# Kernel optimization log

Hardware: AMD Instinct MI355X
Metric: run time of the kernel (lower is better)

## Reference

```python
import jax, jax.numpy as jnp
import numpy as np

NOTRACK_BOX = jnp.array([-1.0, -1.0, -1.0, -1.0], dtype=jnp.float32)
ROI_SIZE = 7


def make_boxes(key, B, N):
    k1, k2 = jax.random.split(key)
    lo = jax.random.uniform(k1, (B, N, 2)) * 0.5            # (ymin, xmin)
    sz = jax.random.uniform(k2, (B, N, 2)) * 0.45 + 0.05    # box extent
    hi = jnp.minimum(lo + sz, 1.0)
    boxes = jnp.concatenate([lo, hi], axis=-1)               # [B,N,4] ymin,xmin,ymax,xmax
    # mark last 2 slots per batch as empty (NOTRACK_BOX)
    boxes = boxes.at[:, -2:, :].set(-1.0)
    return boxes


def setup_inputs() -> dict:
    key = jax.random.key(0)
    ks = jax.random.split(key, 6)
    B, H, W, N, C, D = 16, 512, 512, 16, 256, 256
    images = jax.random.normal(ks[0], (B, H, W, 3), dtype=jnp.float32)
    bboxes = make_boxes(ks[1], B, N)
    conv_w = jax.random.normal(ks[2], (16, 16, 3, C), dtype=jnp.float32) * 0.05
    conv_b = jnp.zeros((C,), dtype=jnp.float32)
    dense_w = jax.random.normal(ks[3], (C, D), dtype=jnp.float32) * (1.0 / np.sqrt(C))
    dense_b = jnp.zeros((D,), dtype=jnp.float32)
    return {"images": images, "bboxes": bboxes, "conv_w": conv_w,
            "conv_b": conv_b, "dense_w": dense_w, "dense_b": dense_b}


def backbone(images, conv_w, conv_b):
    # stride-16 conv stem: [B,512,512,3] -> [B,32,32,C]
    feat = jax.lax.conv_general_dilated(
        images, conv_w, window_strides=(16, 16), padding="VALID",
        dimension_numbers=("NHWC", "HWIO", "NHWC"))
    return jax.nn.relu(feat + conv_b)


def roi_align(bboxes, feat, size):
    # bboxes: [B,N,4] normalized (ymin,xmin,ymax,xmax); feat: [B,H,W,C]
    B, H, W, C = feat.shape
    ymin, xmin, ymax, xmax = [bboxes[..., i] for i in range(4)]  # each [B,N]
    steps = (jnp.arange(size, dtype=feat.dtype) + 0.5) / size    # [S]
    ys = ymin[..., None] + (ymax - ymin)[..., None] * steps      # [B,N,S]
    xs = xmin[..., None] + (xmax - xmin)[..., None] * steps      # [B,N,S]
    py = ys * H - 0.5
    px = xs * W - 0.5
    y0f = jnp.floor(py); x0f = jnp.floor(px)
    wy = py - y0f; wx = px - x0f                                 # [B,N,S]
    y0 = jnp.clip(y0f.astype(jnp.int32), 0, H - 1)
    y1 = jnp.clip(y0f.astype(jnp.int32) + 1, 0, H - 1)
    x0 = jnp.clip(x0f.astype(jnp.int32), 0, W - 1)
    x1 = jnp.clip(x0f.astype(jnp.int32) + 1, 0, W - 1)
    N, S = y0.shape[1], size
    def grid(yi, xi):  # [B,N,S] x [B,N,S] -> [B,N,S,S] index grids
        return (jnp.broadcast_to(yi[:, :, :, None], (B, N, S, S)),
                jnp.broadcast_to(xi[:, :, None, :], (B, N, S, S)))
    gather = jax.vmap(lambda f, yy, xx: f[yy, xx])  # per-batch fancy gather
    def corner(yi, xi):
        yy, xx = grid(yi, xi)
        return gather(feat, yy, xx)                              # [B,N,S,S,C]
    w00 = ((1 - wy)[:, :, :, None] * (1 - wx)[:, :, None, :])[..., None]
    w01 = ((1 - wy)[:, :, :, None] * wx[:, :, None, :])[..., None]
    w10 = (wy[:, :, :, None] * (1 - wx)[:, :, None, :])[..., None]
    w11 = (wy[:, :, :, None] * wx[:, :, None, :])[..., None]
    return (w00 * corner(y0, x0) + w01 * corner(y0, x1)
            + w10 * corner(y1, x0) + w11 * corner(y1, x1))        # [B,N,S,S,C]


def reference(images, bboxes, conv_w, conv_b, dense_w, dense_b):
    bboxes = jax.lax.stop_gradient(bboxes)
    feat = backbone(images, conv_w, conv_b)                      # [B,32,32,C]
    roi = roi_align(bboxes, feat, ROI_SIZE)                      # [B,N,S,S,C]
    obj = jnp.mean(roi, axis=(-3, -2))                           # [B,N,C] (mean aggregate)
    is_non_empty = jnp.any(bboxes != NOTRACK_BOX, axis=-1, keepdims=True)
    obj = jnp.where(is_non_empty, obj, jnp.zeros_like(obj))
    return obj @ dense_w + dense_b                               # [B,N,D]
```

## Files before the change

kernel.cpp:

```cpp
#include <hip/hip_runtime.h>
#include <hip/hip_bf16.h>

typedef __attribute__((ext_vector_type(8))) short bf16x8;
typedef __attribute__((ext_vector_type(4))) float f32x4;
typedef __attribute__((ext_vector_type(4))) int i32x4;

__device__ inline unsigned int pack_bf2(float a, float b) {
    unsigned int ua = __builtin_bit_cast(unsigned int, a);
    unsigned int ub = __builtin_bit_cast(unsigned int, b);
    ua = (ua + 0x7fffu + ((ua >> 16) & 1u)) >> 16;
    ub = (ub + 0x7fffu + ((ub >> 16) & 1u)) >> 16;
    return (ub << 16) | (ua & 0xffffu);
}

__global__ void pack_w_kernel(const float* __restrict__ conv_w, i32x4* __restrict__ bpack) {
    int t = blockIdx.x * 256 + threadIdx.x;
    int lane = t & 63;
    int g = t >> 6;
    int nt = g / 24, ks = g - nt * 24;
    int k0 = ks * 32 + ((lane >> 4) << 3);
    int n  = nt * 16 + (lane & 15);
    const float* src = conv_w + (size_t)k0 * 256 + n;
    float v[8];
#pragma unroll
    for (int j = 0; j < 8; ++j) v[j] = src[(size_t)j * 256];
    i32x4 o;
    o.x = pack_bf2(v[0], v[1]);
    o.y = pack_bf2(v[2], v[3]);
    o.z = pack_bf2(v[4], v[5]);
    o.w = pack_bf2(v[6], v[7]);
    bpack[t] = o;
}

__global__ __launch_bounds__(512) void conv_kernel(
    const float* __restrict__ images,
    const i32x4* __restrict__ bpack,
    const float* __restrict__ conv_b,
    float* __restrict__ feat) {
    __shared__ short ldsA[2][64 * 104];

    const int tid  = threadIdx.x;
    const int lane = tid & 63;
    const int w    = tid >> 6;
    const int l15  = lane & 15;
    const int lg   = lane >> 4;
    const int wr   = w >> 2;
    const int wc   = w & 3;

    const int work  = (blockIdx.x & 7) * 64 + (blockIdx.x >> 3);
    const int mi    = work >> 1;
    const int nhalf = work & 1;

    const int ss = tid >> 8;
    const int sr = (tid >> 7) & 1;
    const int tc = tid & 127;
    const int gstrip = 2 * mi + ss;
    const float* rowbase = images
        + (size_t)(((gstrip >> 5) << 9) + ((gstrip & 31) << 4) + sr) * 1536 + tc * 4;

    int widx[3];
#pragma unroll
    for (int p = 0; p < 3; ++p) {
        int fp = tc + (p << 7);
        int j = (fp * 1366) >> 14;
        int q = fp - 12 * j;
        widx[p] = (ss * 32 + j) * 104 + sr * 48 + (q << 2);
    }

    float bias[2];
#pragma unroll
    for (int sub = 0; sub < 2; ++sub)
        bias[sub] = conv_b[nhalf * 128 + wc * 32 + sub * 16 + l15];

    const i32x4* bp = bpack + (size_t)((nhalf * 8 + wc * 2) * 24) * 64 + lane;

    f32x4 acc[2][2] = {};
    f32x4 st[3];

#pragma unroll
    for (int p = 0; p < 3; ++p) st[p] = *(const f32x4*)(rowbase + p * 512);
#pragma unroll
    for (int p = 0; p < 3; ++p) {
        int2 v;
        v.x = pack_bf2(st[p].x, st[p].y);
        v.y = pack_bf2(st[p].z, st[p].w);
        *(int2*)(&ldsA[0][widx[p]]) = v;
    }
    __syncthreads();

#pragma unroll
    for (int c = 0; c < 8; ++c) {
        i32x4 Bc[2][3];
#pragma unroll
        for (int sub = 0; sub < 2; ++sub)
#pragma unroll
        for (int s = 0; s < 3; ++s)
            Bc[sub][s] = bp[(size_t)(sub * 24 + c * 3 + s) * 64];
        if (c < 7) {
            const float* rb = rowbase + (size_t)(c + 1) * 3072;
#pragma unroll
            for (int p = 0; p < 3; ++p) st[p] = *(const f32x4*)(rb + p * 512);
        }
        const short* bufA = &ldsA[c & 1][0];
#pragma unroll
        for (int s = 0; s < 3; ++s) {
            bf16x8 aF0 = *(const bf16x8*)(&bufA[(wr * 32 + l15) * 104 + s * 32 + lg * 8]);
            bf16x8 aF1 = *(const bf16x8*)(&bufA[(wr * 32 + 16 + l15) * 104 + s * 32 + lg * 8]);
#pragma unroll
            for (int sub = 0; sub < 2; ++sub) {
                bf16x8 bF = __builtin_bit_cast(bf16x8, Bc[sub][s]);
                acc[0][sub] = __builtin_amdgcn_mfma_f32_16x16x32_bf16(aF0, bF, acc[0][sub], 0, 0, 0);
                acc[1][sub] = __builtin_amdgcn_mfma_f32_16x16x32_bf16(aF1, bF, acc[1][sub], 0, 0, 0);
            }
        }
        if (c < 7) {
            short* dstA = &ldsA[(c + 1) & 1][0];
#pragma unroll
            for (int p = 0; p < 3; ++p) {
                int2 v;
                v.x = pack_bf2(st[p].x, st[p].y);
                v.y = pack_bf2(st[p].z, st[p].w);
                *(int2*)(&dstA[widx[p]]) = v;
            }
        }
        __syncthreads();
    }

    const int m0 = mi * 64 + wr * 32;
    const int nc0 = nhalf * 128 + wc * 32;
#pragma unroll
    for (int mt = 0; mt < 2; ++mt)
#pragma unroll
    for (int sub = 0; sub < 2; ++sub)
#pragma unroll
    for (int r = 0; r < 4; ++r) {
        int m = m0 + mt * 16 + lg * 4 + r;
        float v = acc[mt][sub][r] + bias[sub];
        feat[(size_t)m * 256 + nc0 + sub * 16 + l15] = fmaxf(v, 0.f);
    }
}

__global__ __launch_bounds__(512) void roi_dense_kernel(
    const float* __restrict__ bboxes,
    const float* __restrict__ feat,
    const float* __restrict__ dense_w,
    const float* __restrict__ dense_b,
    float* __restrict__ out) {
    __shared__ int   offs[4][49];
    __shared__ float wts[4][49];
    __shared__ float part[512];
    __shared__ float objv[256];

    const int bn = blockIdx.x;
    const int b  = bn >> 4;
    const int tid = threadIdx.x;

    const float4 box = *(const float4*)(bboxes + (size_t)bn * 4);
    bool empty = (box.x == -1.f) & (box.y == -1.f) & (box.z == -1.f) & (box.w == -1.f);
    if (empty) {
        if (tid < 256) out[(size_t)bn * 256 + tid] = dense_b[tid];
        return;
    }

    if (tid < 49) {
        int sy = tid / 7, sx = tid - sy * 7;
        float py = (box.x + (box.z - box.x) * ((sy + 0.5f) * (1.0f / 7.0f))) * 32.f - 0.5f;
        float px = (box.y + (box.w - box.y) * ((sx + 0.5f) * (1.0f / 7.0f))) * 32.f - 0.5f;
        float y0f = floorf(py), x0f = floorf(px);
        float wy = py - y0f, wx = px - x0f;
        int y0 = min(max((int)y0f, 0), 31);
        int y1 = min(max((int)y0f + 1, 0), 31);
        int x0 = min(max((int)x0f, 0), 31);
        int x1 = min(max((int)x0f + 1, 0), 31);
        offs[0][tid] = (y0 * 32 + x0) * 256;
        offs[1][tid] = (y0 * 32 + x1) * 256;
        offs[2][tid] = (y1 * 32 + x0) * 256;
        offs[3][tid] = (y1 * 32 + x1) * 256;
        wts[0][tid] = (1.f - wy) * (1.f - wx);
        wts[1][tid] = (1.f - wy) * wx;
        wts[2][tid] = wy * (1.f - wx);
        wts[3][tid] = wy * wx;
    }
    __syncthreads();

    const int c = tid & 255, h = tid >> 8;
    const float* fb = feat + (size_t)b * (1024 * 256) + c;
    float accv = 0.f;
    for (int s = h; s < 49; s += 2) {
        accv += wts[0][s] * fb[offs[0][s]];
        accv += wts[1][s] * fb[offs[1][s]];
        accv += wts[2][s] * fb[offs[2][s]];
        accv += wts[3][s] * fb[offs[3][s]];
    }
    part[tid] = accv;
    __syncthreads();
    if (tid < 256) objv[tid] = (part[tid] + part[tid + 256]) * (1.f / 49.f);
    __syncthreads();

    const float* dwp = dense_w + (size_t)(h * 128) * 256 + c;
    float da = 0.f;
#pragma unroll 8
    for (int cc = 0; cc < 128; ++cc) da += objv[h * 128 + cc] * dwp[(size_t)cc * 256];
    part[tid] = da;
    __syncthreads();
    if (tid < 256) out[(size_t)bn * 256 + tid] = part[tid] + part[tid + 256] + dense_b[tid];
}

extern "C" void kernel_launch(void* const* d_in, const int* in_sizes, int n_in,
                              void* d_out, int out_size, void* d_ws, size_t ws_size,
                              hipStream_t stream) {
    const float* images  = (const float*)d_in[0];
    const float* bboxes  = (const float*)d_in[1];
    const float* conv_w  = (const float*)d_in[2];
    const float* conv_b  = (const float*)d_in[3];
    const float* dense_w = (const float*)d_in[4];
    const float* dense_b = (const float*)d_in[5];
    float* out = (float*)d_out;

    char* ws = (char*)d_ws;
    i32x4* bpack = (i32x4*)ws;
    float* feat  = (float*)(ws + 512 * 1024);

    pack_w_kernel<<<96, 256, 0, stream>>>(conv_w, bpack);
    conv_kernel<<<512, 512, 0, stream>>>(images, bpack, conv_b, feat);
    roi_dense_kernel<<<256, 512, 0, stream>>>(bboxes, feat, dense_w, dense_b, out);
}
```

Before: 40.43 us.

## Retile conv so each block covers one feature row across all channels; store bf16 features

The conv kernel now gives each block one 32-pixel output row across all 256 channels, instead of 64 rows by 128 channels. Each image strip is therefore loaded once, not twice across two channel halves. The K loop is restructured into 4 chunks of 4 image rows with two register staging sets, and each chunk holds more K steps between barriers. The feature map is also written and read as bf16, which halves intermediate traffic for the ROI gather at the cost of an extra rounding of the features.

```diff
diff --git a/kernel.cpp b/kernel.cpp
--- a/kernel.cpp
+++ b/kernel.cpp
@@ -11,6 +11,14 @@
     ua = (ua + 0x7fffu + ((ua >> 16) & 1u)) >> 16;
     ub = (ub + 0x7fffu + ((ub >> 16) & 1u)) >> 16;
     return (ub << 16) | (ua & 0xffffu);
+}
+__device__ inline unsigned short f2bf1(float a) {
+    unsigned int u = __builtin_bit_cast(unsigned int, a);
+    u = (u + 0x7fffu + ((u >> 16) & 1u)) >> 16;
+    return (unsigned short)u;
+}
+__device__ inline float bf2f(unsigned short u) {
+    return __builtin_bit_cast(float, ((unsigned int)u) << 16);
 }
 
 __global__ void pack_w_kernel(const float* __restrict__ conv_w, i32x4* __restrict__ bpack) {
@@ -36,76 +44,78 @@
     const float* __restrict__ images,
     const i32x4* __restrict__ bpack,
     const float* __restrict__ conv_b,
-    float* __restrict__ feat) {
-    __shared__ short ldsA[2][64 * 104];
+    unsigned short* __restrict__ featB) {
+    __shared__ short ldsA[2][32 * 200];
 
     const int tid  = threadIdx.x;
     const int lane = tid & 63;
     const int w    = tid >> 6;
     const int l15  = lane & 15;
     const int lg   = lane >> 4;
-    const int wr   = w >> 2;
-    const int wc   = w & 3;
-
-    const int work  = (blockIdx.x & 7) * 64 + (blockIdx.x >> 3);
-    const int mi    = work >> 1;
-    const int nhalf = work & 1;
-
-    const int ss = tid >> 8;
-    const int sr = (tid >> 7) & 1;
+
+    const int g = blockIdx.x;
+    const int b = g >> 5, ii = g & 31;
+
+    const int sr = tid >> 7;
     const int tc = tid & 127;
-    const int gstrip = 2 * mi + ss;
-    const float* rowbase = images
-        + (size_t)(((gstrip >> 5) << 9) + ((gstrip & 31) << 4) + sr) * 1536 + tc * 4;
+    const float* rowb = images + (size_t)(b * 512 + ii * 16 + sr) * 1536 + tc * 4;
 
     int widx[3];
 #pragma unroll
     for (int p = 0; p < 3; ++p) {
-        int fp = tc + (p << 7);
-        int j = (fp * 1366) >> 14;
-        int q = fp - 12 * j;
-        widx[p] = (ss * 32 + j) * 104 + sr * 48 + (q << 2);
+        int f0 = tc * 4 + p * 512;
+        int j = f0 / 48;
+        int off = f0 - 48 * j;
+        widx[p] = j * 200 + sr * 48 + off;
     }
 
     float bias[2];
 #pragma unroll
     for (int sub = 0; sub < 2; ++sub)
-        bias[sub] = conv_b[nhalf * 128 + wc * 32 + sub * 16 + l15];
-
-    const i32x4* bp = bpack + (size_t)((nhalf * 8 + wc * 2) * 24) * 64 + lane;
+        bias[sub] = conv_b[w * 32 + sub * 16 + l15];
+
+    const i32x4* bp = bpack + (size_t)(2 * w * 24) * 64 + lane;
 
     f32x4 acc[2][2] = {};
-    f32x4 st[3];
-
-#pragma unroll
-    for (int p = 0; p < 3; ++p) st[p] = *(const f32x4*)(rowbase + p * 512);
-#pragma unroll
-    for (int p = 0; p < 3; ++p) {
-        int2 v;
-        v.x = pack_bf2(st[p].x, st[p].y);
-        v.y = pack_bf2(st[p].z, st[p].w);
-        *(int2*)(&ldsA[0][widx[p]]) = v;
-    }
-    __syncthreads();
-
-#pragma unroll
-    for (int c = 0; c < 8; ++c) {
-        i32x4 Bc[2][3];
+    f32x4 ldS0[3], ldS1[3];
+
+    {
+        f32x4 t0[3];
+#pragma unroll
+        for (int p = 0; p < 3; ++p) t0[p] = *(const f32x4*)(rowb + p * 512);
+#pragma unroll
+        for (int p = 0; p < 3; ++p) ldS1[p] = *(const f32x4*)(rowb + 4 * 1536 + p * 512);
+#pragma unroll
+        for (int p = 0; p < 3; ++p) {
+            int2 v;
+            v.x = pack_bf2(t0[p].x, t0[p].y);
+            v.y = pack_bf2(t0[p].z, t0[p].w);
+            *(int2*)(&ldsA[0][widx[p]]) = v;
+        }
+    }
+    __syncthreads();
+
+#pragma unroll
+    for (int rc = 0; rc < 4; ++rc) {
+        i32x4 Bc[2][6];
 #pragma unroll
         for (int sub = 0; sub < 2; ++sub)
 #pragma unroll
-        for (int s = 0; s < 3; ++s)
-            Bc[sub][s] = bp[(size_t)(sub * 24 + c * 3 + s) * 64];
-        if (c < 7) {
-            const float* rb = rowbase + (size_t)(c + 1) * 3072;
-#pragma unroll
-            for (int p = 0; p < 3; ++p) st[p] = *(const f32x4*)(rb + p * 512);
-        }
-        const short* bufA = &ldsA[c & 1][0];
-#pragma unroll
-        for (int s = 0; s < 3; ++s) {
-            bf16x8 aF0 = *(const bf16x8*)(&bufA[(wr * 32 + l15) * 104 + s * 32 + lg * 8]);
-            bf16x8 aF1 = *(const bf16x8*)(&bufA[(wr * 32 + 16 + l15) * 104 + s * 32 + lg * 8]);
+        for (int s = 0; s < 6; ++s)
+            Bc[sub][s] = bp[(size_t)(sub * 24 + rc * 6 + s) * 64];
+        if (rc == 0) {
+#pragma unroll
+            for (int p = 0; p < 3; ++p) ldS0[p] = *(const f32x4*)(rowb + 8 * 1536 + p * 512);
+        }
+        if (rc == 1) {
+#pragma unroll
+            for (int p = 0; p < 3; ++p) ldS1[p] = *(const f32x4*)(rowb + 12 * 1536 + p * 512);
+        }
+        const short* bufA = &ldsA[rc & 1][0];
+#pragma unroll
+        for (int s = 0; s < 6; ++s) {
+            bf16x8 aF0 = *(const bf16x8*)(&bufA[l15 * 200 + s * 32 + lg * 8]);
+            bf16x8 aF1 = *(const bf16x8*)(&bufA[(16 + l15) * 200 + s * 32 + lg * 8]);
 #pragma unroll
             for (int sub = 0; sub < 2; ++sub) {
                 bf16x8 bF = __builtin_bit_cast(bf16x8, Bc[sub][s]);
@@ -113,21 +123,30 @@
                 acc[1][sub] = __builtin_amdgcn_mfma_f32_16x16x32_bf16(aF1, bF, acc[1][sub], 0, 0, 0);
             }
         }
-        if (c < 7) {
-            short* dstA = &ldsA[(c + 1) & 1][0];
-#pragma unroll
-            for (int p = 0; p < 3; ++p) {
-                int2 v;
-                v.x = pack_bf2(st[p].x, st[p].y);
-                v.y = pack_bf2(st[p].z, st[p].w);
-                *(int2*)(&dstA[widx[p]]) = v;
+        if (rc < 3) {
+            short* dst = &ldsA[(rc + 1) & 1][0];
+            if ((rc & 1) == 0) {
+#pragma unroll
+                for (int p = 0; p < 3; ++p) {
+                    int2 v;
+                    v.x = pack_bf2(ldS1[p].x, ldS1[p].y);
+                    v.y = pack_bf2(ldS1[p].z, ldS1[p].w);
+                    *(int2*)(&dst[widx[p]]) = v;
+                }
+            } else {
+#pragma unroll
+                for (int p = 0; p < 3; ++p) {
+                    int2 v;
+                    v.x = pack_bf2(ldS0[p].x, ldS0[p].y);
+                    v.y = pack_bf2(ldS0[p].z, ldS0[p].w);
+                    *(int2*)(&dst[widx[p]]) = v;
+                }
             }
         }
         __syncthreads();
     }
 
-    const int m0 = mi * 64 + wr * 32;
-    const int nc0 = nhalf * 128 + wc * 32;
+    const int m0 = g * 32;
 #pragma unroll
     for (int mt = 0; mt < 2; ++mt)
 #pragma unroll
@@ -135,14 +154,15 @@
 #pragma unroll
     for (int r = 0; r < 4; ++r) {
         int m = m0 + mt * 16 + lg * 4 + r;
+        int n = w * 32 + sub * 16 + l15;
         float v = acc[mt][sub][r] + bias[sub];
-        feat[(size_t)m * 256 + nc0 + sub * 16 + l15] = fmaxf(v, 0.f);
+        featB[(size_t)m * 256 + n] = f2bf1(fmaxf(v, 0.f));
     }
 }
 
 __global__ __launch_bounds__(512) void roi_dense_kernel(
     const float* __restrict__ bboxes,
-    const float* __restrict__ feat,
+    const unsigned short* __restrict__ featB,
     const float* __restrict__ dense_w,
     const float* __restrict__ dense_b,
     float* __restrict__ out) {
@@ -184,13 +204,13 @@
     __syncthreads();
 
     const int c = tid & 255, h = tid >> 8;
-    const float* fb = feat + (size_t)b * (1024 * 256) + c;
+    const unsigned short* fb = featB + (size_t)b * (1024 * 256) + c;
     float accv = 0.f;
     for (int s = h; s < 49; s += 2) {
-        accv += wts[0][s] * fb[offs[0][s]];
-        accv += wts[1][s] * fb[offs[1][s]];
-        accv += wts[2][s] * fb[offs[2][s]];
-        accv += wts[3][s] * fb[offs[3][s]];
+        accv += wts[0][s] * bf2f(fb[offs[0][s]]);
+        accv += wts[1][s] * bf2f(fb[offs[1][s]]);
+        accv += wts[2][s] * bf2f(fb[offs[2][s]]);
+        accv += wts[3][s] * bf2f(fb[offs[3][s]]);
     }
     part[tid] = accv;
     __syncthreads();
@@ -219,9 +239,9 @@
 
     char* ws = (char*)d_ws;
     i32x4* bpack = (i32x4*)ws;
-    float* feat  = (float*)(ws + 512 * 1024);
+    unsigned short* featB = (unsigned short*)(ws + 512 * 1024);
 
     pack_w_kernel<<<96, 256, 0, stream>>>(conv_w, bpack);
-    conv_kernel<<<512, 512, 0, stream>>>(images, bpack, conv_b, feat);
-    roi_dense_kernel<<<256, 512, 0, stream>>>(bboxes, feat, dense_w, dense_b, out);
-}
+    conv_kernel<<<512, 512, 0, stream>>>(images, bpack, conv_b, featB);
+    roi_dense_kernel<<<256, 512, 0, stream>>>(bboxes, featB, dense_w, dense_b, out);
+}
```

Result: faster. 39.35 us (-2.7%).
